# Kernel tuning notes

Measured on AMD Instinct MI355X. Metric: run time of the kernel, lower is better.

The kernel has to match this reference:

```python
import math
import jax, jax.numpy as jnp
import numpy as np

SR = 44100
N_HARMONICS = 64
EPS = 1e-5
LOG10 = math.log(10.0)


def scale_function(x):
    # ddsp_pytorch util.scale_function: 2 * sigmoid(x)**log(10) + 1e-7
    return 2.0 * jax.nn.sigmoid(x) ** LOG10 + 1e-7


def setup_inputs() -> dict:
    key = jax.random.key(0)
    k1, k2, k3 = jax.random.split(key, 3)
    bs, n_samples = 32, 64000
    # f0 in [80, 480] Hz so upper harmonics cross Nyquist for some frames
    f0_hz = jax.random.uniform(k1, (bs, n_samples), dtype=jnp.float32) * 400.0 + 80.0
    harmonic_amplitudes = jax.random.normal(k2, (bs, n_samples, N_HARMONICS + 1), dtype=jnp.float32)
    phase = jax.random.uniform(k3, (bs,), dtype=jnp.float32) * 2.0 * jnp.pi
    return {"f0_hz": f0_hz, "harmonic_amplitudes": harmonic_amplitudes, "phase": phase}


def reference(f0_hz, harmonic_amplitudes, phase):
    ha = scale_function(harmonic_amplitudes)            # (bs, S, H+1)
    f0 = f0_hz[..., None]                               # (bs, S, 1)
    total_amplitude = ha[..., :1]                       # (bs, S, 1)
    ha = ha[..., 1:]                                    # (bs, S, H)
    harm = jnp.arange(1, N_HARMONICS + 1, dtype=f0.dtype)  # (H,)
    # anti-alias: zero harmonics above Nyquist
    aa = (f0 * harm < SR / 2).astype(f0.dtype)
    ha_aa = ha * aa
    ha_aa = ha_aa / (jnp.sum(ha_aa, axis=-1, keepdims=True) + EPS)
    ha_aa = ha_aa * total_amplitude
    # phase integration
    omega = jnp.cumsum(2.0 * jnp.pi * f0 / SR, axis=1)  # (bs, S, 1)
    omega = omega + phase.reshape(-1, 1, 1)
    omegas = omega * harm                               # (bs, S, H)
    signal = jnp.sum(jnp.sin(omegas) * ha_aa, axis=-1)  # (bs, S)
    return signal
```

## Files before the change

kernel.cpp:

```cpp
#include <hip/hip_runtime.h>
#include <math.h>

#define BATCH    32
#define CHUNK    128
#define NCHUNK   500
#define NCH_TOT  (BATCH * NCHUNK)
#define TAB_N    1152
#define PBLOCKS  512

__device__ __forceinline__ float scale_fn(float x) {
    float e = exp2f(-1.4426950408889634f * x);
    float l = log2f(1.0f + e);
    return 2.0f * exp2f(-2.302585092994046f * l) + 1e-7f;
}

#define GLOAD_LDS16(g, l)  __builtin_amdgcn_global_load_lds(                 \
    (const __attribute__((address_space(1))) void*)(g),                      \
    (__attribute__((address_space(3))) void*)(l), 16, 0, 0)

__global__ __launch_bounds__(128) void table_kernel(float* __restrict__ gtab) {
    int i = blockIdx.x * 128 + threadIdx.x;
    if (i < TAB_N) gtab[i] = scale_fn(fmaf((float)i, 0.015625f, -8.0f));
}

__global__ __launch_bounds__(128) void chunk_sum_kernel(
        const float* __restrict__ f0, double* __restrict__ csum) {
    int bx = blockIdx.x;
    int t  = threadIdx.x;
    double v = (double)f0[(long)bx * CHUNK + t];
    for (int off = 32; off > 0; off >>= 1) v += __shfl_down(v, off, 64);
    __shared__ double ws[2];
    if ((t & 63) == 0) ws[t >> 6] = v;
    __syncthreads();
    if (t == 0) csum[bx] = ws[0] + ws[1];
}

__global__ __launch_bounds__(512) void chunk_scan_kernel(double* __restrict__ csum) {
    int r = blockIdx.x;
    int t = threadIdx.x;
    int lane = t & 63, w = t >> 6;
    double orig = (t < NCHUNK) ? csum[(long)r * NCHUNK + t] : 0.0;
    double v = orig;
    for (int off = 1; off < 64; off <<= 1) {
        double n = __shfl_up(v, off, 64);
        if (lane >= off) v += n;
    }
    __shared__ double wsum[8];
    if (lane == 63) wsum[w] = v;
    __syncthreads();
    double add = 0.0;
    for (int i = 0; i < w; ++i) add += wsum[i];
    v += add;
    if (t < NCHUNK) csum[(long)r * NCHUNK + t] = v - orig;
}

__global__ __launch_bounds__(128) void nu_kernel(
        const float* __restrict__ f0, const double* __restrict__ csum,
        const float* __restrict__ phase, float* __restrict__ nuarr) {
    int bx = blockIdx.x;
    int r  = bx / NCHUNK;
    int t  = threadIdx.x;
    int lane = t & 63, w = t >> 6;
    long sbase = (long)bx * CHUNK;
    double v = (double)f0[sbase + t];
    for (int off = 1; off < 64; off <<= 1) {
        double n = __shfl_up(v, off, 64);
        if (lane >= off) v += n;
    }
    __shared__ double wsum[2];
    if (lane == 63) wsum[w] = v;
    __syncthreads();
    if (w == 1) v += wsum[0];
    v += csum[bx];
    double x = v * (1.0 / 44100.0) + (double)phase[r] * 0.15915494309189535;
    x -= floor(x);
    nuarr[sbase + t] = (float)x;
}

__global__ __launch_bounds__(512, 4) void osc_kernel(
        const float* __restrict__ f0,
        const float* __restrict__ ha,
        const float* __restrict__ nuarr,
        const float* __restrict__ gtab,
        float* __restrict__ out) {
    int b = blockIdx.x;
    int t = threadIdx.x;
    int lane = t & 63, w = t >> 6;

    __shared__ float slab[2][CHUNK * 65];
    __shared__ float tab[TAB_N];

    if (t < 288) ((float4*)tab)[t] = ((const float4*)gtab)[t];

    int nIter = (b < (NCH_TOT - 31 * PBLOCKS)) ? 32 : 31;

    auto stage = [&](int buf, int c) {
        const char* src = (const char*)ha + (long)c * (CHUNK * 65 * 4);
        char*       dst = (char*)slab[buf];
        #pragma unroll
        for (int k = 0; k < 4; ++k) {
            int rr = w + 8 * k;
            GLOAD_LDS16(src + rr * 1024 + lane * 16,
                        dst + rr * 1024 + lane * 16);
        }
        if (w == 0)
            GLOAD_LDS16(src + 32256 + lane * 16,
                        dst + 32256 + lane * 16);
    };

    stage(0, b);

    for (int i = 0; i < nIter; ++i) {
        int c = i * PBLOCKS + b;
        __syncthreads();
        if (i + 1 < nIter) stage((i + 1) & 1, c + PBLOCKS);

        const float* amp = slab[i & 1];
        long sbase = (long)c * CHUNK;
        int s  = w * 16 + (lane & 15);
        int q  = lane >> 4;
        int h0 = q * 16;

        float f0v = f0[sbase + s];
        float nu  = nuarr[sbase + s];

        float k0 = floorf(22050.0f / f0v);
        if (f0v * (k0 + 1.0f) < 22050.0f)      k0 += 1.0f;
        else if (!(f0v * k0 < 22050.0f))       k0 -= 1.0f;

        float c2;
        {
            float th = 6.283185307179586f * nu;
            c2 = 2.0f * __cosf(th);
        }
        float m1 = (float)(h0 + 1) * nu; m1 -= floorf(m1);
        float m2 = (float)(h0 + 2) * nu; m2 -= floorf(m2);
        float sA = __sinf(6.283185307179586f * m1);
        float sB = __sinf(6.283185307179586f * m2);

        const float* arow = amp + s * 65 + 1 + h0;

        float S1 = 0.0f, S2 = 0.0f;
        #pragma unroll
        for (int j = 0; j < 16; j += 2) {
            float a0 = arow[j];
            float a1 = arow[j + 1];
            float tc0 = fmaf(a0, 64.0f, 512.0f);
            tc0 = fminf(fmaxf(tc0, 0.0f), 1022.99f);
            float fi0 = floorf(tc0); int i0 = (int)fi0; float fr0 = tc0 - fi0;
            float w0 = fmaf(fr0, tab[i0 + 1] - tab[i0], tab[i0]);
            float tc1 = fmaf(a1, 64.0f, 512.0f);
            tc1 = fminf(fmaxf(tc1, 0.0f), 1022.99f);
            float fi1 = floorf(tc1); int i1 = (int)fi1; float fr1 = tc1 - fi1;
            float w1 = fmaf(fr1, tab[i1 + 1] - tab[i1], tab[i1]);

            w0 = ((float)(h0 + 1 + j) <= k0) ? w0 : 0.0f;
            w1 = ((float)(h0 + 2 + j) <= k0) ? w1 : 0.0f;

            S1 += w0; S2 = fmaf(w0, sA, S2);
            S1 += w1; S2 = fmaf(w1, sB, S2);

            float sn1 = fmaf(c2, sB, -sA);
            float sn2 = fmaf(c2, sn1, -sB);
            sA = sn1; sB = sn2;
        }

        S1 += __shfl_xor(S1, 16, 64);
        S1 += __shfl_xor(S1, 32, 64);
        S2 += __shfl_xor(S2, 16, 64);
        S2 += __shfl_xor(S2, 32, 64);

        if (q == 0) {
            float total = scale_fn(amp[s * 65]);
            out[sbase + s] = total * S2 / (S1 + 1e-5f);
        }
    }
}

extern "C" void kernel_launch(void* const* d_in, const int* in_sizes, int n_in,
                              void* d_out, int out_size, void* d_ws, size_t ws_size,
                              hipStream_t stream) {
    (void)in_sizes; (void)n_in; (void)out_size; (void)ws_size;
    const float* f0    = (const float*)d_in[0];
    const float* ha    = (const float*)d_in[1];
    const float* phase = (const float*)d_in[2];
    float* out = (float*)d_out;

    double* csum = (double*)d_ws;
    float*  gtab = (float*)((char*)d_ws + 131072);
    float*  nuarr = (float*)((char*)d_ws + 262144);

    table_kernel<<<(TAB_N + 127) / 128, 128, 0, stream>>>(gtab);
    chunk_sum_kernel<<<NCH_TOT, CHUNK, 0, stream>>>(f0, csum);
    chunk_scan_kernel<<<BATCH, 512, 0, stream>>>(csum);
    nu_kernel<<<NCH_TOT, CHUNK, 0, stream>>>(f0, csum, phase, nuarr);
    osc_kernel<<<PBLOCKS, 512, 0, stream>>>(f0, ha, nuarr, gtab, out);
}
```

Before: 678.6 us.

## Replace persistent double-buffered osc kernel with one block per chunk reading global directly

```diff
diff --git a/kernel.cpp b/kernel.cpp
--- a/kernel.cpp
+++ b/kernel.cpp
@@ -1,26 +1,17 @@
 #include <hip/hip_runtime.h>
 #include <math.h>
+
 
 #define BATCH    32
 #define CHUNK    128
 #define NCHUNK   500
 #define NCH_TOT  (BATCH * NCHUNK)
 #define TAB_N    1152
-#define PBLOCKS  512
 
 __device__ __forceinline__ float scale_fn(float x) {
     float e = exp2f(-1.4426950408889634f * x);
     float l = log2f(1.0f + e);
     return 2.0f * exp2f(-2.302585092994046f * l) + 1e-7f;
-}
-
-#define GLOAD_LDS16(g, l)  __builtin_amdgcn_global_load_lds(                 \
-    (const __attribute__((address_space(1))) void*)(g),                      \
-    (__attribute__((address_space(3))) void*)(l), 16, 0, 0)
-
-__global__ __launch_bounds__(128) void table_kernel(float* __restrict__ gtab) {
-    int i = blockIdx.x * 128 + threadIdx.x;
-    if (i < TAB_N) gtab[i] = scale_fn(fmaf((float)i, 0.015625f, -8.0f));
 }
 
 __global__ __launch_bounds__(128) void chunk_sum_kernel(
@@ -77,103 +68,76 @@
     nuarr[sbase + t] = (float)x;
 }
 
-__global__ __launch_bounds__(512, 4) void osc_kernel(
+__global__ __launch_bounds__(512) void osc_kernel(
         const float* __restrict__ f0,
         const float* __restrict__ ha,
         const float* __restrict__ nuarr,
-        const float* __restrict__ gtab,
         float* __restrict__ out) {
-    int b = blockIdx.x;
+    int c = blockIdx.x;
     int t = threadIdx.x;
     int lane = t & 63, w = t >> 6;
 
-    __shared__ float slab[2][CHUNK * 65];
     __shared__ float tab[TAB_N];
 
-    if (t < 288) ((float4*)tab)[t] = ((const float4*)gtab)[t];
+    long sbase = (long)c * CHUNK;
+    int s  = w * 16 + (lane >> 2);
+    int q  = lane & 3;
+    int h0 = q * 16;
 
-    int nIter = (b < (NCH_TOT - 31 * PBLOCKS)) ? 32 : 31;
+    float f0v = f0[sbase + s];
+    float nu  = nuarr[sbase + s];
 
-    auto stage = [&](int buf, int c) {
-        const char* src = (const char*)ha + (long)c * (CHUNK * 65 * 4);
-        char*       dst = (char*)slab[buf];
-        #pragma unroll
-        for (int k = 0; k < 4; ++k) {
-            int rr = w + 8 * k;
-            GLOAD_LDS16(src + rr * 1024 + lane * 16,
-                        dst + rr * 1024 + lane * 16);
-        }
-        if (w == 0)
-            GLOAD_LDS16(src + 32256 + lane * 16,
-                        dst + 32256 + lane * 16);
-    };
+    tab[t]       = scale_fn(fmaf((float)t,          0.015625f, -8.0f));
+    tab[t + 512] = scale_fn(fmaf((float)(t + 512),  0.015625f, -8.0f));
+    if (t < TAB_N - 1024)
+        tab[t + 1024] = scale_fn(fmaf((float)(t + 1024), 0.015625f, -8.0f));
+    __syncthreads();
 
-    stage(0, b);
+    float k0 = floorf(22050.0f / f0v);
+    if (f0v * (k0 + 1.0f) < 22050.0f)      k0 += 1.0f;
+    else if (!(f0v * k0 < 22050.0f))       k0 -= 1.0f;
 
-    for (int i = 0; i < nIter; ++i) {
-        int c = i * PBLOCKS + b;
-        __syncthreads();
-        if (i + 1 < nIter) stage((i + 1) & 1, c + PBLOCKS);
+    float c2 = 2.0f * __cosf(6.283185307179586f * nu);
+    float m1 = (float)(h0 + 1) * nu; m1 -= floorf(m1);
+    float m2 = (float)(h0 + 2) * nu; m2 -= floorf(m2);
+    float sA = __sinf(6.283185307179586f * m1);
+    float sB = __sinf(6.283185307179586f * m2);
 
-        const float* amp = slab[i & 1];
-        long sbase = (long)c * CHUNK;
-        int s  = w * 16 + (lane & 15);
-        int q  = lane >> 4;
-        int h0 = q * 16;
+    const float* __restrict__ arow = ha + (sbase + s) * 65 + 1 + h0;
 
-        float f0v = f0[sbase + s];
-        float nu  = nuarr[sbase + s];
+    float S1 = 0.0f, S2 = 0.0f;
+    #pragma unroll
+    for (int j = 0; j < 16; j += 2) {
+        float a0 = arow[j];
+        float a1 = arow[j + 1];
+        float tc0 = fmaf(a0, 64.0f, 512.0f);
+        tc0 = fminf(fmaxf(tc0, 0.0f), 1022.99f);
+        float fi0 = floorf(tc0); int i0 = (int)fi0; float fr0 = tc0 - fi0;
+        float w0 = fmaf(fr0, tab[i0 + 1] - tab[i0], tab[i0]);
+        float tc1 = fmaf(a1, 64.0f, 512.0f);
+        tc1 = fminf(fmaxf(tc1, 0.0f), 1022.99f);
+        float fi1 = floorf(tc1); int i1 = (int)fi1; float fr1 = tc1 - fi1;
+        float w1 = fmaf(fr1, tab[i1 + 1] - tab[i1], tab[i1]);
 
-        float k0 = floorf(22050.0f / f0v);
-        if (f0v * (k0 + 1.0f) < 22050.0f)      k0 += 1.0f;
-        else if (!(f0v * k0 < 22050.0f))       k0 -= 1.0f;
+        w0 = ((float)(h0 + 1 + j) <= k0) ? w0 : 0.0f;
+        w1 = ((float)(h0 + 2 + j) <= k0) ? w1 : 0.0f;
 
-        float c2;
-        {
-            float th = 6.283185307179586f * nu;
-            c2 = 2.0f * __cosf(th);
-        }
-        float m1 = (float)(h0 + 1) * nu; m1 -= floorf(m1);
-        float m2 = (float)(h0 + 2) * nu; m2 -= floorf(m2);
-        float sA = __sinf(6.283185307179586f * m1);
-        float sB = __sinf(6.283185307179586f * m2);
+        S1 += w0; S2 = fmaf(w0, sA, S2);
+        S1 += w1; S2 = fmaf(w1, sB, S2);
 
-        const float* arow = amp + s * 65 + 1 + h0;
+        float sn1 = fmaf(c2, sB, -sA);
+        float sn2 = fmaf(c2, sn1, -sB);
+        sA = sn1; sB = sn2;
+    }
 
-        float S1 = 0.0f, S2 = 0.0f;
-        #pragma unroll
-        for (int j = 0; j < 16; j += 2) {
-            float a0 = arow[j];
-            float a1 = arow[j + 1];
-            float tc0 = fmaf(a0, 64.0f, 512.0f);
-            tc0 = fminf(fmaxf(tc0, 0.0f), 1022.99f);
-            float fi0 = floorf(tc0); int i0 = (int)fi0; float fr0 = tc0 - fi0;
-            float w0 = fmaf(fr0, tab[i0 + 1] - tab[i0], tab[i0]);
-            float tc1 = fmaf(a1, 64.0f, 512.0f);
-            tc1 = fminf(fmaxf(tc1, 0.0f), 1022.99f);
-            float fi1 = floorf(tc1); int i1 = (int)fi1; float fr1 = tc1 - fi1;
-            float w1 = fmaf(fr1, tab[i1 + 1] - tab[i1], tab[i1]);
+    S1 += __shfl_xor(S1, 1, 64);
+    S1 += __shfl_xor(S1, 2, 64);
+    S2 += __shfl_xor(S2, 1, 64);
+    S2 += __shfl_xor(S2, 2, 64);
 
-            w0 = ((float)(h0 + 1 + j) <= k0) ? w0 : 0.0f;
-            w1 = ((float)(h0 + 2 + j) <= k0) ? w1 : 0.0f;
-
-            S1 += w0; S2 = fmaf(w0, sA, S2);
-            S1 += w1; S2 = fmaf(w1, sB, S2);
-
-            float sn1 = fmaf(c2, sB, -sA);
-            float sn2 = fmaf(c2, sn1, -sB);
-            sA = sn1; sB = sn2;
-        }
-
-        S1 += __shfl_xor(S1, 16, 64);
-        S1 += __shfl_xor(S1, 32, 64);
-        S2 += __shfl_xor(S2, 16, 64);
-        S2 += __shfl_xor(S2, 32, 64);
-
-        if (q == 0) {
-            float total = scale_fn(amp[s * 65]);
-            out[sbase + s] = total * S2 / (S1 + 1e-5f);
-        }
+    if (q == 0) {
+        float total = scale_fn(ha[(sbase + s) * 65]);
+        out[sbase + s] = total * S2 / (S1 + 1e-5f);
     }
 }
 
@@ -186,13 +150,11 @@
     const float* phase = (const float*)d_in[2];
     float* out = (float*)d_out;
 
-    double* csum = (double*)d_ws;
-    float*  gtab = (float*)((char*)d_ws + 131072);
+    double* csum  = (double*)d_ws;
     float*  nuarr = (float*)((char*)d_ws + 262144);
 
-    table_kernel<<<(TAB_N + 127) / 128, 128, 0, stream>>>(gtab);
     chunk_sum_kernel<<<NCH_TOT, CHUNK, 0, stream>>>(f0, csum);
     chunk_scan_kernel<<<BATCH, 512, 0, stream>>>(csum);
     nu_kernel<<<NCH_TOT, CHUNK, 0, stream>>>(f0, csum, phase, nuarr);
-    osc_kernel<<<PBLOCKS, 512, 0, stream>>>(f0, ha, nuarr, gtab, out);
+    osc_kernel<<<NCH_TOT, 512, 0, stream>>>(f0, ha, nuarr, out);
 }
```

Result: slower. 698.6 us (+3.0%).
